# Kernel tuning notes

Measured on AMD Instinct MI355X. Metric: run time of the kernel, lower is better.

The kernel has to match this reference:

```python
import jax, jax.numpy as jnp
import numpy as np
import math

H = 8        # num_heads
D = 32       # dim_head
DEPTH = 1
LAMBDA_INIT = 0.8 - 0.6 * math.exp(-0.3 * DEPTH)
EPS = 1e-8


def setup_inputs() -> dict:
    key = jax.random.key(0)
    ks = jax.random.split(key, 9)
    B, T, IN_DIM, OUT_DIM = 2, 2048, 1024, 1024
    E = 2 * H * D  # 512
    inp = {
        "x": jax.random.normal(ks[0], (B, T, IN_DIM), dtype=jnp.float32),
        "Wq": jax.random.normal(ks[1], (IN_DIM, E), dtype=jnp.float32) * (IN_DIM ** -0.5),
        "Wkv": jax.random.normal(ks[2], (IN_DIM, 2 * E), dtype=jnp.float32) * (IN_DIM ** -0.5),
        "Wout": jax.random.normal(ks[3], (E, OUT_DIM), dtype=jnp.float32) * (E ** -0.5),
        "lambda_q1": 0.1 * jax.random.normal(ks[4], (D,), dtype=jnp.float32),
        "lambda_k1": 0.1 * jax.random.normal(ks[5], (D,), dtype=jnp.float32),
        "lambda_q2": 0.1 * jax.random.normal(ks[6], (D,), dtype=jnp.float32),
        "lambda_k2": 0.1 * jax.random.normal(ks[7], (D,), dtype=jnp.float32),
        "gamma": jnp.ones((2 * D,), dtype=jnp.float32),
    }
    return inp


def reference(x, Wq, Wkv, Wout, lambda_q1, lambda_k1, lambda_q2, lambda_k2, gamma):
    B, T, _ = x.shape
    scaling = D ** -0.5

    q = (x @ Wq).reshape(B, T, 2 * H, D).transpose(0, 2, 1, 3) * scaling  # [B,2H,T,D]
    kv = x @ Wkv
    k, v = jnp.split(kv, 2, axis=-1)
    k = k.reshape(B, T, 2 * H, D).transpose(0, 2, 1, 3)        # [B,2H,T,D]
    v = v.reshape(B, T, H, 2 * D).transpose(0, 2, 1, 3)        # [B,H,T,2D]

    dots = jnp.einsum('bhqd,bhkd->bhqk', q, k)                 # [B,2H,T,T]
    attn_w = jax.nn.softmax(dots.astype(jnp.float32), axis=-1).astype(dots.dtype)

    lam1 = jnp.exp(jnp.sum(lambda_q1 * lambda_k1))
    lam2 = jnp.exp(jnp.sum(lambda_q2 * lambda_k2))
    lam = lam1 - lam2 + LAMBDA_INIT

    attn_w = attn_w.reshape(B, H, 2, T, T)
    attn_w = attn_w[:, :, 0] - lam * attn_w[:, :, 1]           # [B,H,T,T]

    attn = jnp.einsum('bhqk,bhkd->bhqd', attn_w, v)            # [B,H,T,2D]

    rms = jnp.sqrt(jnp.mean(attn * attn, axis=-1, keepdims=True))
    attn = gamma * (attn / (rms + EPS))
    attn = attn * (1.0 - LAMBDA_INIT)

    attn = attn.transpose(0, 2, 1, 3).reshape(B, T, 2 * H * D)  # [B,T,E]
    return attn @ Wout
```

## Files before the change

### kernel.cpp

```cpp
#include <hip/hip_runtime.h>

typedef __attribute__((ext_vector_type(8)))  _Float16 half8;
typedef __attribute__((ext_vector_type(4)))  _Float16 half4;
typedef __attribute__((ext_vector_type(2)))  __fp16   fp16x2;
typedef __attribute__((ext_vector_type(4)))  float    f32x4;

#define MFMA16(a,b,c) __builtin_amdgcn_mfma_f32_16x16x32_f16(a,b,c,0,0,0)

#define QSCALE       0.17677669529663687f
#define LAMBDA_INIT  0.3555090675909693f
#define OUT_SCALE    0.6444909324090307f
#define LOG2E        1.4426950408889634f
#define MSHIFT       4.0f

#define EXP2(x) __builtin_amdgcn_exp2f(x)

__device__ __forceinline__ void gld16(const void* g, void* l) {
    __builtin_amdgcn_global_load_lds(
        (const __attribute__((address_space(1))) unsigned int*)g,
        (__attribute__((address_space(3))) unsigned int*)l, 16, 0, 0);
}

__device__ __forceinline__ void tr64(const float* __restrict__ src,
                                     _Float16* __restrict__ dst,
                                     int srcld, int dstld, int bx, int by) {
    __shared__ float t[64][65];
    int k0 = bx * 64, n0 = by * 64;
    int c = threadIdx.x & 63, rr = threadIdx.x >> 6;
#pragma unroll
    for (int ph = 0; ph < 16; ++ph) {
        int k = ph * 4 + rr;
        t[k][c] = src[(size_t)(k0 + k) * srcld + n0 + c];
    }
    __syncthreads();
#pragma unroll
    for (int ph = 0; ph < 16; ++ph) {
        int n = ph * 4 + rr;
        dst[(size_t)(n0 + n) * dstld + k0 + c] = (_Float16)t[c][n];
    }
}

__global__ __launch_bounds__(256) void k_prep(const float* __restrict__ x,
                                              const float* __restrict__ Wq,
                                              const float* __restrict__ Wkv,
                                              const float* __restrict__ Wout,
                                              _Float16* __restrict__ xh,
                                              _Float16* __restrict__ WallT,
                                              _Float16* __restrict__ WoutT) {
    int b = blockIdx.x;
    if (b < 4096) {
        int i = (b * 256 + threadIdx.x) * 4;
        f32x4 v = *(const f32x4*)(x + i);
        half4 h;
        h[0] = (_Float16)v[0]; h[1] = (_Float16)v[1];
        h[2] = (_Float16)v[2]; h[3] = (_Float16)v[3];
        *(half4*)(xh + i) = h;
    } else if (b < 4224) {
        int idx = b - 4096;
        tr64(Wq, WallT, 512, 1024, idx & 15, idx >> 4);
    } else if (b < 4480) {
        int idx = b - 4224;
        tr64(Wkv, WallT + 512 * 1024, 1024, 1024, idx & 15, idx >> 4);
    } else {
        int idx = b - 4480;
        tr64(Wout, WoutT, 1024, 512, idx & 7, idx >> 3);
    }
}

__device__ __forceinline__ void gemm_loop(const _Float16* __restrict__ A,
                                          const _Float16* __restrict__ Bt,
                                          int K, int bm, int bn,
                                          char* As, char* Bs,
                                          f32x4 (&acc)[4][4]) {
    int tid = threadIdx.x, lane = tid & 63, w = tid >> 6;
    int col16 = lane & 15, quad = lane >> 4;
    int wm = (w >> 1) << 6, wn = (w & 1) << 6;
    int r0 = tid >> 2;
    int kc = (tid & 3) << 3;
    const _Float16* ga0 = A  + (size_t)(bm + r0) * K + kc;
    const _Float16* ga1 = A  + (size_t)(bm + 64 + r0) * K + kc;
    const _Float16* gb0 = Bt + (size_t)(bn + r0) * K + kc;
    const _Float16* gb1 = Bt + (size_t)(bn + 64 + r0) * K + kc;
    char* lA = As + (w << 10);
    char* lB = Bs + (w << 10);

    for (int k0 = 0; k0 < K; k0 += 32) {
        __syncthreads();
        gld16(ga0 + k0, lA);
        gld16(ga1 + k0, lA + 4096);
        gld16(gb0 + k0, lB);
        gld16(gb1 + k0, lB + 4096);
        __syncthreads();
        half8 af[4], bf[4];
#pragma unroll
        for (int i = 0; i < 4; ++i)
            af[i] = *(const half8*)(As + ((wm + i * 16 + col16) << 6) + (quad << 4));
#pragma unroll
        for (int j = 0; j < 4; ++j)
            bf[j] = *(const half8*)(Bs + ((wn + j * 16 + col16) << 6) + (quad << 4));
#pragma unroll
        for (int i = 0; i < 4; ++i)
#pragma unroll
            for (int j = 0; j < 4; ++j)
                acc[i][j] = MFMA16(af[i], bf[j], acc[i][j]);
    }
}

__global__ __launch_bounds__(256) void k_gemm_qkv(const _Float16* __restrict__ xh,
                                                  const _Float16* __restrict__ WallT,
                                                  _Float16* __restrict__ qbuf,
                                                  char* __restrict__ Kf,
                                                  char* __restrict__ Vf) {
    __shared__ __align__(16) char As[8192];
    __shared__ __align__(16) char Bs[8192];
    f32x4 acc[4][4] = {};
    int bm = blockIdx.x * 128, bn = blockIdx.y * 128;
    gemm_loop(xh, WallT, 1024, bm, bn, As, Bs, acc);

    int tid = threadIdx.x, lane = tid & 63, w = tid >> 6;
    int col16 = lane & 15, quad = lane >> 4;
    int wm = (w >> 1) << 6, wn = (w & 1) << 6;

    if (bn < 512) {
        const float s = QSCALE * LOG2E;
#pragma unroll
        for (int i = 0; i < 4; ++i)
#pragma unroll
            for (int j = 0; j < 4; ++j) {
                int n = bn + wn + j * 16 + col16;
                int m0 = bm + wm + i * 16 + quad * 4;
#pragma unroll
                for (int r = 0; r < 4; ++r)
                    qbuf[(size_t)(m0 + r) * 512 + n] = (_Float16)(acc[i][j][r] * s);
            }
    } else if (bn < 1024) {
#pragma unroll
        for (int j = 0; j < 4; ++j) {
            int n = bn + wn + j * 16 + col16 - 512;
            int pp = n >> 6, dd = n & 63, head = dd >> 5, d32 = dd & 31;
            int lbase = (d32 >> 3) << 4;
            int e2 = (d32 & 7) << 1;
            int fragb = head << 11;
#pragma unroll
            for (int i = 0; i < 4; ++i) {
                int m0 = bm + wm + i * 16 + quad * 4;
                int b = m0 >> 11, tok = m0 & 2047, kb = tok >> 5, kk = tok & 31;
                char* dst = Kf + (((size_t)((b * 8 + pp) * 64 + kb)) << 12)
                          + fragb + ((kk >> 4) << 10) + ((lbase + (kk & 15)) << 4) + e2;
#pragma unroll
                for (int r = 0; r < 4; ++r)
                    *(_Float16*)(dst + (r << 4)) = (_Float16)acc[i][j][r];
            }
        }
    } else {
#pragma unroll
        for (int j = 0; j < 4; ++j) {
            int n = bn + wn + j * 16 + col16 - 1024;
            int pp = n >> 6, ch = n & 63;
            int off_t = ((ch >> 4) << 10) + ((ch & 15) << 4);
#pragma unroll
            for (int i = 0; i < 4; ++i) {
                int m0 = bm + wm + i * 16 + quad * 4;
                int b = m0 >> 11, tok = m0 & 2047, kb = tok >> 5, kk = tok & 31;
                int quadv = (kk < 16) ? (kk >> 2) : ((kk - 16) >> 2);
                int e0 = (kk < 16) ? 0 : 4;
                half4 hv;
#pragma unroll
                for (int r = 0; r < 4; ++r) hv[r] = (_Float16)acc[i][j][r];
                *(half4*)(Vf + (((size_t)((b * 8 + pp) * 64 + kb)) << 12)
                          + off_t + (quadv << 8) + (e0 << 1)) = hv;
            }
        }
    }
}

__global__ __launch_bounds__(256) void k_attn(const _Float16* __restrict__ qbuf,
                                              const char* __restrict__ Kf,
                                              const char* __restrict__ Vf,
                                              _Float16* __restrict__ Po,
                                              float* __restrict__ Pl,
                                              int nc) {
    __shared__ __align__(16) char Sh[32768];

    int blk = blockIdx.x;
    int qt = blk & 31, p = (blk >> 5) & 7, bb = (blk >> 8) & 1, c = blk >> 9;
    int tid = threadIdx.x, lane = tid & 63, w = tid >> 6;
    int col16 = lane & 15, quad = lane >> 4;
    int iters = 32 / nc;

    int qrow = bb * 2048 + qt * 64 + w * 16 + col16;
    const _Float16* qb = qbuf + (size_t)qrow * 512 + p * 64;
    half8 q1 = *(const half8*)(qb + quad * 8);
    half8 q2 = *(const half8*)(qb + 32 + quad * 8);

    size_t choff = (size_t)c * ((size_t)iters << 13);
    const char* Kb = Kf + (((size_t)(bb * 8 + p)) << 18) + choff;
    const char* Vb = Vf + (((size_t)(bb * 8 + p)) << 18) + choff;
    const f32x4 minit = {-MSHIFT, -MSHIFT, -MSHIFT, -MSHIFT};
    int t16 = tid << 4;

    float l1 = 0.f, l2 = 0.f;
    f32x4 o1[4] = {}, o2[4] = {};
    {
        gld16(Kb + t16, Sh + t16);          gld16(Kb + 4096 + t16, Sh + 4096 + t16);
        gld16(Vb + t16, Sh + 8192 + t16);   gld16(Vb + 4096 + t16, Sh + 12288 + t16);
    }
    for (int it = 0; it < iters; ++it) {
        __syncthreads();
        const char* cur = Sh + ((it & 1) << 14);
        if (it + 1 < iters) {
            const char* sk = Kb + ((size_t)(it + 1) << 13);
            const char* sv = Vb + ((size_t)(it + 1) << 13);
            char* d = Sh + (((it + 1) & 1) << 14);
            gld16(sk + t16, d + t16);          gld16(sk + 4096 + t16, d + 4096 + t16);
            gld16(sv + t16, d + 8192 + t16);   gld16(sv + 4096 + t16, d + 12288 + t16);
        }
#pragma unroll
        for (int g = 0; g < 2; ++g) {
            const char* kbase = cur + (g << 12) + (lane << 4);
            const char* vbase = cur + 8192 + (g << 12) + (lane << 4);
            half8 kf0 = *(const half8*)(kbase);
            half8 kf1 = *(const half8*)(kbase + 1024);
            half8 kf2 = *(const half8*)(kbase + 2048);
            half8 kf3 = *(const half8*)(kbase + 3072);
            f32x4 sa1 = MFMA16(kf0, q1, minit), sb1 = MFMA16(kf1, q1, minit);
            f32x4 sa2 = MFMA16(kf2, q2, minit), sb2 = MFMA16(kf3, q2, minit);

            union { half8 v; fp16x2 h[4]; } p1u, p2u;
            {
                float a0 = EXP2(sa1[0]), a1 = EXP2(sa1[1]);
                float a2 = EXP2(sa1[2]), a3 = EXP2(sa1[3]);
                float b0 = EXP2(sb1[0]), b1 = EXP2(sb1[1]);
                float b2 = EXP2(sb1[2]), b3 = EXP2(sb1[3]);
                l1 += ((a0 + a1) + (a2 + a3)) + ((b0 + b1) + (b2 + b3));
                p1u.h[0] = __builtin_amdgcn_cvt_pkrtz(a0, a1);
                p1u.h[1] = __builtin_amdgcn_cvt_pkrtz(a2, a3);
                p1u.h[2] = __builtin_amdgcn_cvt_pkrtz(b0, b1);
                p1u.h[3] = __builtin_amdgcn_cvt_pkrtz(b2, b3);
            }
            {
                float a0 = EXP2(sa2[0]), a1 = EXP2(sa2[1]);
                float a2 = EXP2(sa2[2]), a3 = EXP2(sa2[3]);
                float b0 = EXP2(sb2[0]), b1 = EXP2(sb2[1]);
                float b2 = EXP2(sb2[2]), b3 = EXP2(sb2[3]);
                l2 += ((a0 + a1) + (a2 + a3)) + ((b0 + b1) + (b2 + b3));
                p2u.h[0] = __builtin_amdgcn_cvt_pkrtz(a0, a1);
                p2u.h[1] = __builtin_amdgcn_cvt_pkrtz(a2, a3);
                p2u.h[2] = __builtin_amdgcn_cvt_pkrtz(b0, b1);
                p2u.h[3] = __builtin_amdgcn_cvt_pkrtz(b2, b3);
            }
            half8 vf0 = *(const half8*)(vbase);
            half8 vf1 = *(const half8*)(vbase + 1024);
            half8 vf2 = *(const half8*)(vbase + 2048);
            half8 vf3 = *(const half8*)(vbase + 3072);
            o1[0] = MFMA16(p1u.v, vf0, o1[0]); o2[0] = MFMA16(p2u.v, vf0, o2[0]);
            o1[1] = MFMA16(p1u.v, vf1, o1[1]); o2[1] = MFMA16(p2u.v, vf1, o2[1]);
            o1[2] = MFMA16(p1u.v, vf2, o1[2]); o2[2] = MFMA16(p2u.v, vf2, o2[2]);
            o1[3] = MFMA16(p1u.v, vf3, o1[3]); o2[3] = MFMA16(p2u.v, vf3, o2[3]);
        }
    }
    l1 += __shfl_xor(l1, 16); l1 += __shfl_xor(l1, 32);
    l2 += __shfl_xor(l2, 16); l2 += __shfl_xor(l2, 32);

    int rowbase = (bb * 8 + p) * 2048 + qt * 64 + w * 16;
    _Float16* PoC = Po + (size_t)c * 4194304 + (size_t)rowbase * 128;
#pragma unroll
    for (int r = 0; r < 4; ++r) {
        int rl = quad * 4 + r;
        _Float16* dst = PoC + (size_t)rl * 128 + col16;
#pragma unroll
        for (int t = 0; t < 4; ++t) {
            dst[t * 16]      = (_Float16)o1[t][r];
            dst[64 + t * 16] = (_Float16)o2[t][r];
        }
    }
    if (quad == 0) {
        int idx = rowbase + col16;
        Pl[c * 65536 + idx]         = l1;
        Pl[c * 65536 + 32768 + idx] = l2;
    }
}

__global__ __launch_bounds__(256) void k_combine(const _Float16* __restrict__ Po,
                                                 const float* __restrict__ Pl,
                                                 const float* __restrict__ lq1,
                                                 const float* __restrict__ lk1,
                                                 const float* __restrict__ lq2,
                                                 const float* __restrict__ lk2,
                                                 const float* __restrict__ gamma,
                                                 _Float16* __restrict__ attnO,
                                                 int nc) {
    int gid = blockIdx.x * 256 + threadIdx.x;
    int idx = gid >> 4, j = gid & 15;

    float s1 = 0.f, s2 = 0.f;
#pragma unroll
    for (int i = 0; i < 32; ++i) { s1 += lq1[i] * lk1[i]; s2 += lq2[i] * lk2[i]; }
    float lam = __expf(s1) - __expf(s2) + LAMBDA_INIT;

    size_t rb = (size_t)idx * 128 + j * 4;
    float l1 = 0.f, l2 = 0.f;
    float o1[4] = {}, o2[4] = {};
    for (int c = 0; c < nc; ++c) {
        half4 c1 = *(const half4*)(Po + (size_t)c * 4194304 + rb);
        half4 c2 = *(const half4*)(Po + (size_t)c * 4194304 + rb + 64);
        l1 += Pl[c * 65536 + idx];
        l2 += Pl[c * 65536 + 32768 + idx];
#pragma unroll
        for (int e = 0; e < 4; ++e) { o1[e] += (float)c1[e]; o2[e] += (float)c2[e]; }
    }
    float il1 = 1.f / l1, il2 = lam / l2;
    float Of[4], ss = 0.f;
#pragma unroll
    for (int e = 0; e < 4; ++e) {
        Of[e] = o1[e] * il1 - o2[e] * il2;
        ss += Of[e] * Of[e];
    }
    ss += __shfl_xor(ss, 1, 16); ss += __shfl_xor(ss, 2, 16);
    ss += __shfl_xor(ss, 4, 16); ss += __shfl_xor(ss, 8, 16);
    float rms = sqrtf(ss * 0.015625f);
    float sc = OUT_SCALE / (rms + 1e-8f);

    int b = idx >> 14, p = (idx >> 11) & 7, t = idx & 2047;
    half4 o;
#pragma unroll
    for (int e = 0; e < 4; ++e) o[e] = (_Float16)(gamma[j * 4 + e] * Of[e] * sc);
    *(half4*)(attnO + ((size_t)(b * 2048 + t) * 512) + p * 64 + j * 4) = o;
}

__global__ __launch_bounds__(256) void k_gemm_out(const _Float16* __restrict__ attn,
                                                  const _Float16* __restrict__ WoutT,
                                                  float* __restrict__ out) {
    __shared__ __align__(16) char As[8192];
    __shared__ __align__(16) char Bs[8192];
    f32x4 acc[4][4] = {};
    int bm = blockIdx.x * 128, bn = blockIdx.y * 128;
    gemm_loop(attn, WoutT, 512, bm, bn, As, Bs, acc);

    int tid = threadIdx.x, lane = tid & 63, w = tid >> 6;
    int col16 = lane & 15, quad = lane >> 4;
    int wm = (w >> 1) << 6, wn = (w & 1) << 6;
#pragma unroll
    for (int i = 0; i < 4; ++i)
#pragma unroll
        for (int j = 0; j < 4; ++j) {
            int n = bn + wn + j * 16 + col16;
            int m0 = bm + wm + i * 16 + quad * 4;
#pragma unroll
            for (int r = 0; r < 4; ++r)
                out[(size_t)(m0 + r) * 1024 + n] = acc[i][j][r];
        }
}

extern "C" void kernel_launch(void* const* d_in, const int* in_sizes, int n_in,
                              void* d_out, int out_size, void* d_ws, size_t ws_size,
                              hipStream_t stream) {
    const float* x     = (const float*)d_in[0];
    const float* Wq    = (const float*)d_in[1];
    const float* Wkv   = (const float*)d_in[2];
    const float* Wout  = (const float*)d_in[3];
    const float* lq1   = (const float*)d_in[4];
    const float* lk1   = (const float*)d_in[5];
    const float* lq2   = (const float*)d_in[6];
    const float* lk2   = (const float*)d_in[7];
    const float* gamma = (const float*)d_in[8];
    float* out = (float*)d_out;

    char* ws = (char*)d_ws;
    _Float16* xh    = (_Float16*)(ws);
    _Float16* WallT = (_Float16*)(ws + 8388608);
    float*    Pl    = (float*)(ws + 8388608);
    _Float16* WoutT = (_Float16*)(ws + 11534336);
    _Float16* qbuf  = (_Float16*)(ws + 12582912);
    char*     Kf    = (char*)(ws + 16777216);
    char*     Vf    = (char*)(ws + 20971520);
    _Float16* attn  = (_Float16*)(ws + 25165824);
    _Float16* Po    = (_Float16*)(ws + 29360128);

    int nc = (ws_size >= 62914560u) ? 4 : 1;

    k_prep<<<4608, 256, 0, stream>>>(x, Wq, Wkv, Wout, xh, WallT, WoutT);
    k_gemm_qkv<<<dim3(32, 12), 256, 0, stream>>>(xh, WallT, qbuf, Kf, Vf);
    k_attn<<<nc * 512, 256, 0, stream>>>(qbuf, Kf, Vf, Po, Pl, nc);
    k_combine<<<2048, 256, 0, stream>>>(Po, Pl, lq1, lk1, lq2, lk2, gamma, attn, nc);
    k_gemm_out<<<dim3(32, 8), 256, 0, stream>>>(attn, WoutT, out);
}
```

Before: 180.0 us.

## Read K/V fragments straight from global memory and halve key-split count

Removes the LDS double-buffering of K/V tiles in the attention kernel. Each wave now loads its MFMA fragments directly from global memory (through L1/L2), which drops the __syncthreads barriers and the shared-memory footprint. The iteration count becomes a template parameter, and the key-split factor falls from 4 to 2, which halves the partial outputs the combine kernel must merge but also halves the number of blocks. The risk is that the four waves of a block now each fetch the same K/V from cache instead of sharing one LDS copy, and that fewer blocks give the hardware less parallelism to hide latency.

```diff
diff --git a/kernel.cpp b/kernel.cpp
--- a/kernel.cpp
+++ b/kernel.cpp
@@ -174,55 +174,45 @@
     }
 }
 
+template <int ITERS>
 __global__ __launch_bounds__(256) void k_attn(const _Float16* __restrict__ qbuf,
                                               const char* __restrict__ Kf,
                                               const char* __restrict__ Vf,
                                               _Float16* __restrict__ Po,
-                                              float* __restrict__ Pl,
-                                              int nc) {
-    __shared__ __align__(16) char Sh[32768];
-
+                                              float* __restrict__ Pl) {
     int blk = blockIdx.x;
     int qt = blk & 31, p = (blk >> 5) & 7, bb = (blk >> 8) & 1, c = blk >> 9;
     int tid = threadIdx.x, lane = tid & 63, w = tid >> 6;
     int col16 = lane & 15, quad = lane >> 4;
-    int iters = 32 / nc;
 
     int qrow = bb * 2048 + qt * 64 + w * 16 + col16;
     const _Float16* qb = qbuf + (size_t)qrow * 512 + p * 64;
     half8 q1 = *(const half8*)(qb + quad * 8);
     half8 q2 = *(const half8*)(qb + 32 + quad * 8);
 
-    size_t choff = (size_t)c * ((size_t)iters << 13);
-    const char* Kb = Kf + (((size_t)(bb * 8 + p)) << 18) + choff;
-    const char* Vb = Vf + (((size_t)(bb * 8 + p)) << 18) + choff;
+    size_t choff = (size_t)c * ((size_t)ITERS << 13);
+    const char* Kb = Kf + (((size_t)(bb * 8 + p)) << 18) + choff + (lane << 4);
+    const char* Vb = Vf + (((size_t)(bb * 8 + p)) << 18) + choff + (lane << 4);
     const f32x4 minit = {-MSHIFT, -MSHIFT, -MSHIFT, -MSHIFT};
-    int t16 = tid << 4;
 
     float l1 = 0.f, l2 = 0.f;
     f32x4 o1[4] = {}, o2[4] = {};
-    {
-        gld16(Kb + t16, Sh + t16);          gld16(Kb + 4096 + t16, Sh + 4096 + t16);
-        gld16(Vb + t16, Sh + 8192 + t16);   gld16(Vb + 4096 + t16, Sh + 12288 + t16);
-    }
-    for (int it = 0; it < iters; ++it) {
-        __syncthreads();
-        const char* cur = Sh + ((it & 1) << 14);
-        if (it + 1 < iters) {
-            const char* sk = Kb + ((size_t)(it + 1) << 13);
-            const char* sv = Vb + ((size_t)(it + 1) << 13);
-            char* d = Sh + (((it + 1) & 1) << 14);
-            gld16(sk + t16, d + t16);          gld16(sk + 4096 + t16, d + 4096 + t16);
-            gld16(sv + t16, d + 8192 + t16);   gld16(sv + 4096 + t16, d + 12288 + t16);
-        }
+
+    for (int it = 0; it < ITERS; ++it) {
+        const char* kb = Kb + ((size_t)it << 13);
+        const char* vb = Vb + ((size_t)it << 13);
 #pragma unroll
         for (int g = 0; g < 2; ++g) {
-            const char* kbase = cur + (g << 12) + (lane << 4);
-            const char* vbase = cur + 8192 + (g << 12) + (lane << 4);
+            const char* kbase = kb + (g << 12);
+            const char* vbase = vb + (g << 12);
             half8 kf0 = *(const half8*)(kbase);
             half8 kf1 = *(const half8*)(kbase + 1024);
             half8 kf2 = *(const half8*)(kbase + 2048);
             half8 kf3 = *(const half8*)(kbase + 3072);
+            half8 vf0 = *(const half8*)(vbase);
+            half8 vf1 = *(const half8*)(vbase + 1024);
+            half8 vf2 = *(const half8*)(vbase + 2048);
+            half8 vf3 = *(const half8*)(vbase + 3072);
             f32x4 sa1 = MFMA16(kf0, q1, minit), sb1 = MFMA16(kf1, q1, minit);
             f32x4 sa2 = MFMA16(kf2, q2, minit), sb2 = MFMA16(kf3, q2, minit);
 
@@ -249,10 +239,6 @@
                 p2u.h[2] = __builtin_amdgcn_cvt_pkrtz(b0, b1);
                 p2u.h[3] = __builtin_amdgcn_cvt_pkrtz(b2, b3);
             }
-            half8 vf0 = *(const half8*)(vbase);
-            half8 vf1 = *(const half8*)(vbase + 1024);
-            half8 vf2 = *(const half8*)(vbase + 2048);
-            half8 vf3 = *(const half8*)(vbase + 3072);
             o1[0] = MFMA16(p1u.v, vf0, o1[0]); o2[0] = MFMA16(p2u.v, vf0, o2[0]);
             o1[1] = MFMA16(p1u.v, vf1, o1[1]); o2[1] = MFMA16(p2u.v, vf1, o2[1]);
             o1[2] = MFMA16(p1u.v, vf2, o1[2]); o2[2] = MFMA16(p2u.v, vf2, o2[2]);
@@ -377,11 +363,14 @@
     _Float16* attn  = (_Float16*)(ws + 25165824);
     _Float16* Po    = (_Float16*)(ws + 29360128);
 
-    int nc = (ws_size >= 62914560u) ? 4 : 1;
+    int nc = (ws_size >= 46137344u) ? 2 : 1;
 
     k_prep<<<4608, 256, 0, stream>>>(x, Wq, Wkv, Wout, xh, WallT, WoutT);
     k_gemm_qkv<<<dim3(32, 12), 256, 0, stream>>>(xh, WallT, qbuf, Kf, Vf);
-    k_attn<<<nc * 512, 256, 0, stream>>>(qbuf, Kf, Vf, Po, Pl, nc);
+    if (nc == 2)
+        k_attn<16><<<1024, 256, 0, stream>>>(qbuf, Kf, Vf, Po, Pl);
+    else
+        k_attn<32><<<512, 256, 0, stream>>>(qbuf, Kf, Vf, Po, Pl);
     k_combine<<<2048, 256, 0, stream>>>(Po, Pl, lq1, lk1, lq2, lk2, gamma, attn, nc);
     k_gemm_out<<<dim3(32, 8), 256, 0, stream>>>(attn, WoutT, out);
 }
```

After: 181.2 us. Within noise of the previous version (+0.7%).

## Process two query tiles per attention block and halve the key split count

Applied to the files above, without the earlier changes.

Each attention block now handles 128 query rows (two 64-row sub-tiles) and reuses every K/V tile loaded into shared memory for both sub-tiles. This doubles the MFMA work per LDS load and per barrier. The key dimension is now split two ways instead of four, and the iteration count becomes a template parameter. The grid goes from 2048 to 512 blocks, which lowers occupancy and parallelism. Accumulator register use also doubles.

```diff
diff --git a/kernel.cpp b/kernel.cpp
--- a/kernel.cpp
+++ b/kernel.cpp
@@ -174,41 +174,58 @@
     }
 }
 
+template <int ITERS>
 __global__ __launch_bounds__(256) void k_attn(const _Float16* __restrict__ qbuf,
                                               const char* __restrict__ Kf,
                                               const char* __restrict__ Vf,
                                               _Float16* __restrict__ Po,
-                                              float* __restrict__ Pl,
-                                              int nc) {
+                                              float* __restrict__ Pl) {
     __shared__ __align__(16) char Sh[32768];
 
     int blk = blockIdx.x;
-    int qt = blk & 31, p = (blk >> 5) & 7, bb = (blk >> 8) & 1, c = blk >> 9;
+    int qt = blk & 15, p = (blk >> 4) & 7, bb = (blk >> 7) & 1, c = blk >> 8;
     int tid = threadIdx.x, lane = tid & 63, w = tid >> 6;
     int col16 = lane & 15, quad = lane >> 4;
-    int iters = 32 / nc;
-
-    int qrow = bb * 2048 + qt * 64 + w * 16 + col16;
-    const _Float16* qb = qbuf + (size_t)qrow * 512 + p * 64;
-    half8 q1 = *(const half8*)(qb + quad * 8);
-    half8 q2 = *(const half8*)(qb + 32 + quad * 8);
-
-    size_t choff = (size_t)c * ((size_t)iters << 13);
+
+    int qrow = bb * 2048 + qt * 128 + w * 16 + col16;
+    const _Float16* qba = qbuf + (size_t)qrow * 512 + p * 64;
+    const _Float16* qbb = qba + (size_t)64 * 512;
+    half8 q1a = *(const half8*)(qba + quad * 8);
+    half8 q2a = *(const half8*)(qba + 32 + quad * 8);
+    half8 q1b = *(const half8*)(qbb + quad * 8);
+    half8 q2b = *(const half8*)(qbb + 32 + quad * 8);
+
+    size_t choff = (size_t)c * ((size_t)ITERS << 13);
     const char* Kb = Kf + (((size_t)(bb * 8 + p)) << 18) + choff;
     const char* Vb = Vf + (((size_t)(bb * 8 + p)) << 18) + choff;
     const f32x4 minit = {-MSHIFT, -MSHIFT, -MSHIFT, -MSHIFT};
     int t16 = tid << 4;
 
-    float l1 = 0.f, l2 = 0.f;
-    f32x4 o1[4] = {}, o2[4] = {};
+    float l1a = 0.f, l2a = 0.f, l1b = 0.f, l2b = 0.f;
+    f32x4 oa1[4] = {}, oa2[4] = {}, ob1[4] = {}, ob2[4] = {};
+
+    auto softpack = [&](const f32x4& sa, const f32x4& sb, float& l) -> half8 {
+        union { half8 v; fp16x2 h[4]; } u;
+        float a0 = EXP2(sa[0]), a1 = EXP2(sa[1]);
+        float a2 = EXP2(sa[2]), a3 = EXP2(sa[3]);
+        float b0 = EXP2(sb[0]), b1 = EXP2(sb[1]);
+        float b2 = EXP2(sb[2]), b3 = EXP2(sb[3]);
+        l += ((a0 + a1) + (a2 + a3)) + ((b0 + b1) + (b2 + b3));
+        u.h[0] = __builtin_amdgcn_cvt_pkrtz(a0, a1);
+        u.h[1] = __builtin_amdgcn_cvt_pkrtz(a2, a3);
+        u.h[2] = __builtin_amdgcn_cvt_pkrtz(b0, b1);
+        u.h[3] = __builtin_amdgcn_cvt_pkrtz(b2, b3);
+        return u.v;
+    };
+
     {
         gld16(Kb + t16, Sh + t16);          gld16(Kb + 4096 + t16, Sh + 4096 + t16);
         gld16(Vb + t16, Sh + 8192 + t16);   gld16(Vb + 4096 + t16, Sh + 12288 + t16);
     }
-    for (int it = 0; it < iters; ++it) {
+    for (int it = 0; it < ITERS; ++it) {
         __syncthreads();
         const char* cur = Sh + ((it & 1) << 14);
-        if (it + 1 < iters) {
+        if (it + 1 < ITERS) {
             const char* sk = Kb + ((size_t)(it + 1) << 13);
             const char* sv = Vb + ((size_t)(it + 1) << 13);
             char* d = Sh + (((it + 1) & 1) << 14);
@@ -223,61 +240,57 @@
             half8 kf1 = *(const half8*)(kbase + 1024);
             half8 kf2 = *(const half8*)(kbase + 2048);
             half8 kf3 = *(const half8*)(kbase + 3072);
-            f32x4 sa1 = MFMA16(kf0, q1, minit), sb1 = MFMA16(kf1, q1, minit);
-            f32x4 sa2 = MFMA16(kf2, q2, minit), sb2 = MFMA16(kf3, q2, minit);
-
-            union { half8 v; fp16x2 h[4]; } p1u, p2u;
-            {
-                float a0 = EXP2(sa1[0]), a1 = EXP2(sa1[1]);
-                float a2 = EXP2(sa1[2]), a3 = EXP2(sa1[3]);
-                float b0 = EXP2(sb1[0]), b1 = EXP2(sb1[1]);
-                float b2 = EXP2(sb1[2]), b3 = EXP2(sb1[3]);
-                l1 += ((a0 + a1) + (a2 + a3)) + ((b0 + b1) + (b2 + b3));
-                p1u.h[0] = __builtin_amdgcn_cvt_pkrtz(a0, a1);
-                p1u.h[1] = __builtin_amdgcn_cvt_pkrtz(a2, a3);
-                p1u.h[2] = __builtin_amdgcn_cvt_pkrtz(b0, b1);
-                p1u.h[3] = __builtin_amdgcn_cvt_pkrtz(b2, b3);
-            }
-            {
-                float a0 = EXP2(sa2[0]), a1 = EXP2(sa2[1]);
-                float a2 = EXP2(sa2[2]), a3 = EXP2(sa2[3]);
-                float b0 = EXP2(sb2[0]), b1 = EXP2(sb2[1]);
-                float b2 = EXP2(sb2[2]), b3 = EXP2(sb2[3]);
-                l2 += ((a0 + a1) + (a2 + a3)) + ((b0 + b1) + (b2 + b3));
-                p2u.h[0] = __builtin_amdgcn_cvt_pkrtz(a0, a1);
-                p2u.h[1] = __builtin_amdgcn_cvt_pkrtz(a2, a3);
-                p2u.h[2] = __builtin_amdgcn_cvt_pkrtz(b0, b1);
-                p2u.h[3] = __builtin_amdgcn_cvt_pkrtz(b2, b3);
-            }
+            f32x4 sa1a = MFMA16(kf0, q1a, minit), sb1a = MFMA16(kf1, q1a, minit);
+            f32x4 sa2a = MFMA16(kf2, q2a, minit), sb2a = MFMA16(kf3, q2a, minit);
+            f32x4 sa1b = MFMA16(kf0, q1b, minit), sb1b = MFMA16(kf1, q1b, minit);
+            f32x4 sa2b = MFMA16(kf2, q2b, minit), sb2b = MFMA16(kf3, q2b, minit);
+
+            half8 p1a = softpack(sa1a, sb1a, l1a);
+            half8 p2a = softpack(sa2a, sb2a, l2a);
+            half8 p1b = softpack(sa1b, sb1b, l1b);
+            half8 p2b = softpack(sa2b, sb2b, l2b);
+
             half8 vf0 = *(const half8*)(vbase);
             half8 vf1 = *(const half8*)(vbase + 1024);
             half8 vf2 = *(const half8*)(vbase + 2048);
             half8 vf3 = *(const half8*)(vbase + 3072);
-            o1[0] = MFMA16(p1u.v, vf0, o1[0]); o2[0] = MFMA16(p2u.v, vf0, o2[0]);
-            o1[1] = MFMA16(p1u.v, vf1, o1[1]); o2[1] = MFMA16(p2u.v, vf1, o2[1]);
-            o1[2] = MFMA16(p1u.v, vf2, o1[2]); o2[2] = MFMA16(p2u.v, vf2, o2[2]);
-            o1[3] = MFMA16(p1u.v, vf3, o1[3]); o2[3] = MFMA16(p2u.v, vf3, o2[3]);
-        }
-    }
-    l1 += __shfl_xor(l1, 16); l1 += __shfl_xor(l1, 32);
-    l2 += __shfl_xor(l2, 16); l2 += __shfl_xor(l2, 32);
-
-    int rowbase = (bb * 8 + p) * 2048 + qt * 64 + w * 16;
-    _Float16* PoC = Po + (size_t)c * 4194304 + (size_t)rowbase * 128;
-#pragma unroll
-    for (int r = 0; r < 4; ++r) {
-        int rl = quad * 4 + r;
-        _Float16* dst = PoC + (size_t)rl * 128 + col16;
-#pragma unroll
-        for (int t = 0; t < 4; ++t) {
-            dst[t * 16]      = (_Float16)o1[t][r];
-            dst[64 + t * 16] = (_Float16)o2[t][r];
-        }
-    }
-    if (quad == 0) {
-        int idx = rowbase + col16;
-        Pl[c * 65536 + idx]         = l1;
-        Pl[c * 65536 + 32768 + idx] = l2;
+            oa1[0] = MFMA16(p1a, vf0, oa1[0]); oa2[0] = MFMA16(p2a, vf0, oa2[0]);
+            oa1[1] = MFMA16(p1a, vf1, oa1[1]); oa2[1] = MFMA16(p2a, vf1, oa2[1]);
+            oa1[2] = MFMA16(p1a, vf2, oa1[2]); oa2[2] = MFMA16(p2a, vf2, oa2[2]);
+            oa1[3] = MFMA16(p1a, vf3, oa1[3]); oa2[3] = MFMA16(p2a, vf3, oa2[3]);
+            ob1[0] = MFMA16(p1b, vf0, ob1[0]); ob2[0] = MFMA16(p2b, vf0, ob2[0]);
+            ob1[1] = MFMA16(p1b, vf1, ob1[1]); ob2[1] = MFMA16(p2b, vf1, ob2[1]);
+            ob1[2] = MFMA16(p1b, vf2, ob1[2]); ob2[2] = MFMA16(p2b, vf2, ob2[2]);
+            ob1[3] = MFMA16(p1b, vf3, ob1[3]); ob2[3] = MFMA16(p2b, vf3, ob2[3]);
+        }
+    }
+    l1a += __shfl_xor(l1a, 16); l1a += __shfl_xor(l1a, 32);
+    l2a += __shfl_xor(l2a, 16); l2a += __shfl_xor(l2a, 32);
+    l1b += __shfl_xor(l1b, 16); l1b += __shfl_xor(l1b, 32);
+    l2b += __shfl_xor(l2b, 16); l2b += __shfl_xor(l2b, 32);
+
+    int rowbase = (bb * 8 + p) * 2048 + qt * 128 + w * 16;
+#pragma unroll
+    for (int s = 0; s < 2; ++s) {
+        int rbs = rowbase + s * 64;
+        const f32x4* po1 = s ? ob1 : oa1;
+        const f32x4* po2 = s ? ob2 : oa2;
+        _Float16* PoC = Po + (size_t)c * 4194304 + (size_t)rbs * 128;
+#pragma unroll
+        for (int r = 0; r < 4; ++r) {
+            int rl = quad * 4 + r;
+            _Float16* dst = PoC + (size_t)rl * 128 + col16;
+#pragma unroll
+            for (int t = 0; t < 4; ++t) {
+                dst[t * 16]      = (_Float16)po1[t][r];
+                dst[64 + t * 16] = (_Float16)po2[t][r];
+            }
+        }
+        if (quad == 0) {
+            int idx = rbs + col16;
+            Pl[c * 65536 + idx]         = s ? l1b : l1a;
+            Pl[c * 65536 + 32768 + idx] = s ? l2b : l2a;
+        }
     }
 }
 
@@ -377,11 +390,14 @@
     _Float16* attn  = (_Float16*)(ws + 25165824);
     _Float16* Po    = (_Float16*)(ws + 29360128);
 
-    int nc = (ws_size >= 62914560u) ? 4 : 1;
+    int nc = (ws_size >= 46137344u) ? 2 : 1;
 
     k_prep<<<4608, 256, 0, stream>>>(x, Wq, Wkv, Wout, xh, WallT, WoutT);
     k_gemm_qkv<<<dim3(32, 12), 256, 0, stream>>>(xh, WallT, qbuf, Kf, Vf);
-    k_attn<<<nc * 512, 256, 0, stream>>>(qbuf, Kf, Vf, Po, Pl, nc);
+    if (nc == 2)
+        k_attn<16><<<512, 256, 0, stream>>>(qbuf, Kf, Vf, Po, Pl);
+    else
+        k_attn<32><<<256, 256, 0, stream>>>(qbuf, Kf, Vf, Po, Pl);
     k_combine<<<2048, 256, 0, stream>>>(Po, Pl, lq1, lk1, lq2, lk2, gamma, attn, nc);
     k_gemm_out<<<dim3(32, 8), 256, 0, stream>>>(attn, WoutT, out);
 }
```

Result: faster. 168.9 us (-6.2%).
